# Kernel optimization log

Hardware: AMD Instinct MI355X
Metric: run time of the kernel (lower is better)

The kernel has to match this reference:

```python
import jax, jax.numpy as jnp
import numpy as np
from jax import lax

IN_DIM = 256
MID = IN_DIM // 2          # 128
NUM_FILTERS = 8
OUT_DIM = 256
EMBED_DIM = 256
BN_EPS = 1e-5


def star_relu(x, scale, bias):
    # StarReLU: s * relu(x)**2 + b
    return scale * jnp.square(jax.nn.relu(x)) + bias


def setup_inputs() -> dict:
    key = jax.random.key(0)
    ks = jax.random.split(key, 12)
    B, H, W = 2, 16, 16
    h, w = 128, 128
    inp = {
        "x": jax.random.normal(ks[0], (B, IN_DIM, H, W), jnp.float32),
        "y": jax.random.normal(ks[1], (B, OUT_DIM, h, w), jnp.float32),
        # feature_fuse: 1x1 conv, depthwise 3x3 conv, BatchNorm (eval-mode stats)
        "conv1_w": jax.random.normal(ks[2], (MID, IN_DIM), jnp.float32) * 0.02,
        "conv1_b": jnp.zeros((MID,), jnp.float32),
        "dw_w": jax.random.normal(ks[3], (MID, 3, 3), jnp.float32) * 0.02,
        "dw_b": jnp.zeros((MID,), jnp.float32),
        "bn_gamma": jnp.ones((MID,), jnp.float32),
        "bn_beta": jnp.zeros((MID,), jnp.float32),
        "bn_mean": jax.random.normal(ks[4], (MID,), jnp.float32) * 0.1,
        "bn_var": jax.random.uniform(ks[5], (MID,), jnp.float32, 0.5, 1.5),
        "sr1_scale": jnp.ones((1,), jnp.float32),
        "sr1_bias": jnp.zeros((1,), jnp.float32),
        # channle_expand 1x1 conv
        "ce_w": jax.random.normal(ks[6], (NUM_FILTERS, MID), jnp.float32) * 0.02,
        "ce_b": jnp.zeros((NUM_FILTERS,), jnp.float32),
        "sr2_scale": jnp.ones((1,), jnp.float32),
        "sr2_bias": jnp.zeros((1,), jnp.float32),
        "W_base": jax.random.normal(ks[7], (OUT_DIM * EMBED_DIM, NUM_FILTERS), jnp.float32) * 0.02,
    }
    return inp


def reference(x, y, conv1_w, conv1_b, dw_w, dw_b, bn_gamma, bn_beta, bn_mean,
              bn_var, sr1_scale, sr1_bias, ce_w, ce_b, sr2_scale, sr2_bias, W_base):
    B, _, fh, fw = x.shape
    b, c, h, w = y.shape
    ph, pw = h // fh, w // fw

    # feature_fuse
    t = jnp.einsum('bchw,oc->bohw', x, conv1_w) + conv1_b[None, :, None, None]
    t = lax.conv_general_dilated(
        t, dw_w[:, None, :, :], (1, 1), ((1, 1), (1, 1)),
        feature_group_count=MID,
        dimension_numbers=('NCHW', 'OIHW', 'NCHW')) + dw_b[None, :, None, None]
    t = bn_gamma[None, :, None, None] * (t - bn_mean[None, :, None, None]) \
        * lax.rsqrt(bn_var + BN_EPS)[None, :, None, None] + bn_beta[None, :, None, None]
    t = star_relu(t, sr1_scale, sr1_bias)

    # channle_expand + act -> per-location filter coefficients [b, F, fh, fw]
    wdec = star_relu(jnp.einsum('bchw,fc->bfhw', t, ce_w) + ce_b[None, :, None, None],
                     sr2_scale, sr2_bias)

    # hypernetwork: [b, E*O, fh, fw], flattened as (embed_dim, out_dim)
    Wd = jnp.einsum('bfhw,ef->behw', wdec, W_base)
    Wd = Wd.reshape(b, EMBED_DIM, OUT_DIM, fh, fw)

    # massive-group 1x1 conv == per-(batch, block) small GEMM over spatial patches
    yb = y.reshape(b, c, fh, ph, fw, pw)
    out = jnp.einsum('beoij,boipjq->beipjq', Wd, yb)  # [b, E, fh, ph, fw, pw]
    return out.reshape(b, EMBED_DIM, h, w)
```

## Files before the change

### kernel.cpp

```cpp
#include <hip/hip_runtime.h>
#include <stdint.h>

typedef unsigned short u16t;
typedef unsigned int   u32t;
typedef _Float16       h16;
typedef __attribute__((ext_vector_type(2))) _Float16 h16x2;
typedef __attribute__((ext_vector_type(8))) short short8;
typedef __attribute__((ext_vector_type(4))) float f32x4;

#if defined(__has_builtin)
#if __has_builtin(__builtin_amdgcn_fdot2)
#define HAVE_DOT2 1
#endif
#endif

__device__ __forceinline__ float dot2h(u32t a, u32t b, float c){
#ifdef HAVE_DOT2
  return __builtin_amdgcn_fdot2(__builtin_bit_cast(h16x2, a),
                                __builtin_bit_cast(h16x2, b), c, false);
#else
  h16x2 ha = __builtin_bit_cast(h16x2, a), hb = __builtin_bit_cast(h16x2, b);
  return c + (float)ha[0]*(float)hb[0] + (float)ha[1]*(float)hb[1];
#endif
}

__device__ __forceinline__ float bf2f(u16t h){
  union { u32t u; float f; } c; c.u = ((u32t)h) << 16; return c.f;
}
__device__ __forceinline__ u16t f2bf(float f){
  union { float f; u32t u; } c; c.f = f;
  u32t u = c.u;
  u = u + 0x7fffu + ((u >> 16) & 1u);
  return (u16t)(u >> 16);
}
__device__ __forceinline__ u32t pk2bf(float a, float b){
  return (u32t)f2bf(a) | ((u32t)f2bf(b) << 16);
}
__device__ __forceinline__ u32t pk2h(float a, float b){
  h16x2 h = { (h16)a, (h16)b };
  return __builtin_bit_cast(u32t, h);
}

template<bool BF>
__device__ __forceinline__ float ldv(const void* p, size_t i){
  if constexpr (BF) return bf2f(((const u16t*)p)[i]);
  else              return ((const float*)p)[i];
}
template<bool BF>
__device__ __forceinline__ void ld8(const void* p, size_t i, float* v){
  if constexpr (BF){
    uint4 u = *(const uint4*)((const u16t*)p + i);
    const u32t a[4] = {u.x, u.y, u.z, u.w};
#pragma unroll
    for (int d = 0; d < 4; ++d){
      v[2*d]   = bf2f((u16t)(a[d] & 0xffffu));
      v[2*d+1] = bf2f((u16t)(a[d] >> 16));
    }
  } else {
    const float4* q = (const float4*)((const float*)p + i);
    float4 A = q[0], B = q[1];
    v[0]=A.x; v[1]=A.y; v[2]=A.z; v[3]=A.w;
    v[4]=B.x; v[5]=B.y; v[6]=B.z; v[7]=B.w;
  }
}
template<bool BF>
__device__ __forceinline__ void ld8pk(const void* p, size_t i, u32t* dst){
  if constexpr (BF){
    uint4 u = *(const uint4*)((const u16t*)p + i);
    dst[0]=u.x; dst[1]=u.y; dst[2]=u.z; dst[3]=u.w;
  } else {
    const float4* q = (const float4*)((const float*)p + i);
    float4 A = q[0], B = q[1];
    dst[0] = pk2bf(A.x, A.y); dst[1] = pk2bf(A.z, A.w);
    dst[2] = pk2bf(B.x, B.y); dst[3] = pk2bf(B.z, B.w);
  }
}

__global__ void k_probe(const void* xv, int* flag){
  __shared__ int cnt;
  const int t = threadIdx.x;
  if (t == 0) cnt = 0;
  __syncthreads();
  u16t h = ((const u16t*)xv)[t];
  int e = (h >> 7) & 0xff;
  if (e >= 90 && e <= 150) atomicAdd(&cnt, 1);
  __syncthreads();
  if (t == 0) *flag = (cnt >= 104) ? 1 : 0;
}

template<bool BF>
__device__ __forceinline__ void pre12_body(
    const void* x, const void* w, const void* bias,
    const void* dww, const void* dwb,
    const void* bng, const void* bnb, const void* bnm, const void* bnv,
    const void* s1s, const void* s1b, float* t2)
{
  __shared__ float ts[2][256];
  const int cg = blockIdx.x, b = blockIdx.y;
  const int ij = threadIdx.x, i = ij >> 4, j = ij & 15;
  const int c0 = cg * 2;
  float a0 = ldv<BF>(bias, c0), a1 = ldv<BF>(bias, c0 + 1);
  const size_t xb = (size_t)b * 65536 + ij;
#pragma unroll 8
  for (int k = 0; k < 256; ++k){
    const float xv = ldv<BF>(x, xb + (size_t)k * 256);
    a0 += xv * ldv<BF>(w, (size_t)c0 * 256 + k);
    a1 += xv * ldv<BF>(w, (size_t)(c0 + 1) * 256 + k);
  }
  ts[0][ij] = a0;
  ts[1][ij] = a1;
  __syncthreads();
  const float sc1 = ldv<BF>(s1s, 0), sb1 = ldv<BF>(s1b, 0);
#pragma unroll
  for (int cc = 0; cc < 2; ++cc){
    const int c = c0 + cc;
    float s = ldv<BF>(dwb, c);
#pragma unroll
    for (int di = 0; di < 3; ++di){
      const int ii = i + di - 1;
      if (ii < 0 || ii > 15) continue;
#pragma unroll
      for (int dj = 0; dj < 3; ++dj){
        const int jj = j + dj - 1;
        if (jj < 0 || jj > 15) continue;
        s += ts[cc][ii * 16 + jj] * ldv<BF>(dww, c * 9 + di * 3 + dj);
      }
    }
    const float v = ldv<BF>(bng, c) * (s - ldv<BF>(bnm, c)) *
                    rsqrtf(ldv<BF>(bnv, c) + 1e-5f) + ldv<BF>(bnb, c);
    const float r = fmaxf(v, 0.0f);
    t2[((size_t)b * 128 + c) * 256 + ij] = sc1 * r * r + sb1;
  }
}
__global__ __launch_bounds__(256) void k_pre12(
    const void* x, const void* w, const void* bias,
    const void* dww, const void* dwb,
    const void* bng, const void* bnb, const void* bnm, const void* bnv,
    const void* s1s, const void* s1b, float* t2, const int* flag){
  if (*flag) pre12_body<true >(x,w,bias,dww,dwb,bng,bnb,bnm,bnv,s1s,s1b,t2);
  else       pre12_body<false>(x,w,bias,dww,dwb,bng,bnb,bnm,bnv,s1s,s1b,t2);
}

template<bool BF>
__device__ __forceinline__ void pre3_body(
    const float* t2, const void* cew, const void* ceb,
    const void* s2s, const void* s2b, float* wdecf, uint4* wdech)
{
  const int b = blockIdx.x, ij = threadIdx.x;
  float a[8];
#pragma unroll
  for (int f = 0; f < 8; ++f) a[f] = ldv<BF>(ceb, f);
#pragma unroll 4
  for (int c = 0; c < 128; ++c){
    const float tv = t2[((size_t)b * 128 + c) * 256 + ij];
#pragma unroll
    for (int f = 0; f < 8; ++f) a[f] += tv * ldv<BF>(cew, f * 128 + c);
  }
  const float sc2 = ldv<BF>(s2s, 0), sb2 = ldv<BF>(s2b, 0);
  float o[8];
#pragma unroll
  for (int f = 0; f < 8; ++f){
    const float r = fmaxf(a[f], 0.0f);
    o[f] = sc2 * r * r + sb2;
  }
  const int idx = b * 256 + ij;
#pragma unroll
  for (int f = 0; f < 8; ++f) wdecf[idx * 8 + f] = o[f];
  if (wdech){
    wdech[idx] = make_uint4(pk2h(o[0], o[1]), pk2h(o[2], o[3]),
                            pk2h(o[4], o[5]), pk2h(o[6], o[7]));
  }
}
__global__ __launch_bounds__(256) void k_pre3(
    const float* t2, const void* cew, const void* ceb,
    const void* s2s, const void* s2b, float* wdecf, uint4* wdech, const int* flag){
  if (*flag) pre3_body<true >(t2, cew, ceb, s2s, s2b, wdecf, wdech);
  else       pre3_body<false>(t2, cew, ceb, s2s, s2b, wdecf, wdech);
}

template<bool BF>
__device__ __forceinline__ void prew_body(const void* wb, uint4* wbh){
  const int t = blockIdx.x * 256 + threadIdx.x;
  float v[8];
  ld8<BF>(wb, (size_t)t * 8, v);
  wbh[t] = make_uint4(pk2h(v[0], v[1]), pk2h(v[2], v[3]),
                      pk2h(v[4], v[5]), pk2h(v[6], v[7]));
}
__global__ __launch_bounds__(256) void k_prew(const void* wb, uint4* wbh, const int* flag){
  if (*flag) prew_body<true >(wb, wbh);
  else       prew_body<false>(wb, wbh);
}

template<bool BF, bool PREW>
__device__ __forceinline__ void main_body(
    const void* y, const void* wbase, const uint4* wbh,
    const float* wdecf, const uint4* wdech, void* out, u16t* smem)
{
  const int gx  = blockIdx.x;
  const int ec  = blockIdx.y;
  const int b   = gx >> 6;
  const int i   = (gx >> 2) & 15;
  const int j0  = (gx & 3) * 4;
  const int tid = threadIdx.x;

  {
    const int o_oct = tid & 31;
    const int p     = (tid >> 5) & 7;
    const int gh    = tid >> 8;
#pragma unroll
    for (int gi = 0; gi < 2; ++gi){
      const int g = gh * 2 + gi;
      u32t Rp[8][4];
#pragma unroll
      for (int r = 0; r < 8; ++r){
        const size_t idx = (((size_t)(b * 256 + o_oct * 8 + r)) * 128 + (i * 8 + p)) * 128
                         + (j0 + g) * 8;
        ld8pk<BF>(y, idx, Rp[r]);
      }
#pragma unroll
      for (int q = 0; q < 8; ++q){
        const int d = q >> 1, h = q & 1;
        u32t cc[4];
#pragma unroll
        for (int k = 0; k < 4; ++k){
          const u32t lo32 = Rp[2*k][d], hi32 = Rp[2*k+1][d];
          cc[k] = h ? ((lo32 >> 16)     | (hi32 & 0xffff0000u))
                    : ((lo32 & 0xffffu) | (hi32 << 16));
        }
        const int row  = g * 64 + p * 8 + q;
        const int phys = (o_oct * 8 + row * 8) & 255;
        *(uint4*)(smem + row * 256 + phys) = make_uint4(cc[0], cc[1], cc[2], cc[3]);
      }
    }
  }
  __syncthreads();

  const int wave = tid >> 6, lane = tid & 63;
  const int l15 = lane & 15, l4 = lane >> 4;
  const int e0  = ec * 128 + wave * 16;
  const int e_a = e0 + l15;

  u32t wdp[4][4];
  float wdf[4][8];
#pragma unroll
  for (int g = 0; g < 4; ++g){
    const int loc = b * 256 + i * 16 + j0 + g;
    if constexpr (PREW){
      const uint4 q = wdech[loc];
      wdp[g][0] = q.x; wdp[g][1] = q.y; wdp[g][2] = q.z; wdp[g][3] = q.w;
    } else {
#pragma unroll
      for (int f = 0; f < 8; ++f) wdf[g][f] = wdecf[loc * 8 + f];
    }
  }

  f32x4 acc[4][4];
#pragma unroll
  for (int g = 0; g < 4; ++g)
#pragma unroll
    for (int nt = 0; nt < 4; ++nt)
      acc[g][nt] = (f32x4){0.f, 0.f, 0.f, 0.f};

  const uint4* wb4 = wbh + (size_t)e_a * 256 + l4 * 8;
  const size_t wb_off = (size_t)e_a * 2048 + (size_t)l4 * 64;

  u32t Wb[2][8][4];
#pragma unroll
  for (int m = 0; m < 8; ++m){
    if constexpr (PREW){
      const uint4 q = wb4[m];
      Wb[0][m][0]=q.x; Wb[0][m][1]=q.y; Wb[0][m][2]=q.z; Wb[0][m][3]=q.w;
    } else {
      ld8pk<BF>(wbase, wb_off + m * 8, Wb[0][m]);
    }
  }

#pragma unroll
  for (int ks = 0; ks < 8; ++ks){
    const int cur = ks & 1;
    if (ks < 7){
#pragma unroll
      for (int m = 0; m < 8; ++m){
        if constexpr (PREW){
          const uint4 q = wb4[(ks + 1) * 32 + m];
          Wb[cur^1][m][0]=q.x; Wb[cur^1][m][1]=q.y; Wb[cur^1][m][2]=q.z; Wb[cur^1][m][3]=q.w;
        } else {
          ld8pk<BF>(wbase, wb_off + (size_t)(ks + 1) * 256 + m * 8, Wb[cur^1][m]);
        }
      }
    }
    float s[4][8];
#pragma unroll
    for (int m = 0; m < 8; ++m){
      if constexpr (PREW){
#pragma unroll
        for (int g = 0; g < 4; ++g){
          float t = 0.f;
#pragma unroll
          for (int d = 0; d < 4; ++d) t = dot2h(Wb[cur][m][d], wdp[g][d], t);
          s[g][m] = t;
        }
      } else {
        float wf[8];
#pragma unroll
        for (int d = 0; d < 4; ++d){
          wf[2*d]   = bf2f((u16t)(Wb[cur][m][d] & 0xffffu));
          wf[2*d+1] = bf2f((u16t)(Wb[cur][m][d] >> 16));
        }
#pragma unroll
        for (int g = 0; g < 4; ++g){
          float t = 0.f;
#pragma unroll
          for (int f = 0; f < 8; ++f) t += wf[f] * wdf[g][f];
          s[g][m] = t;
        }
      }
    }
#pragma unroll
    for (int g = 0; g < 4; ++g){
      short8 af;
#pragma unroll
      for (int m = 0; m < 8; ++m) af[m] = (short)f2bf(s[g][m]);
#pragma unroll
      for (int nt = 0; nt < 4; ++nt){
        const int row = g * 64 + nt * 16 + l15;
        const int c0  = (ks * 32 + l4 * 8 + row * 8) & 255;
        const short8 bfr = *(const short8*)(smem + row * 256 + c0);
        acc[g][nt] = __builtin_amdgcn_mfma_f32_16x16x32_bf16(af, bfr, acc[g][nt], 0, 0, 0);
      }
    }
  }

#pragma unroll
  for (int g = 0; g < 4; ++g){
#pragma unroll
    for (int nt = 0; nt < 4; ++nt){
      const int col = nt * 16 + l15;
      const int pp = col >> 3, qq = col & 7;
#pragma unroll
      for (int r = 0; r < 4; ++r){
        const int ee = e0 + l4 * 4 + r;
        const size_t oaddr = ((size_t)(b * 256 + ee) * 128 + (i * 8 + pp)) * 128
                           + (j0 + g) * 8 + qq;
        const float v = acc[g][nt][r];
        if constexpr (BF) ((u16t*)out)[oaddr] = f2bf(v);
        else              ((float*)out)[oaddr] = v;
      }
    }
  }
}

__global__ __launch_bounds__(512, 2) void k_main_pw(
    const void* y, const uint4* wbh, const uint4* wdech, void* out, const int* flag){
  extern __shared__ __align__(16) u16t smem[];
  if (*flag) main_body<true , true>(y, nullptr, wbh, nullptr, wdech, out, smem);
  else       main_body<false, true>(y, nullptr, wbh, nullptr, wdech, out, smem);
}
__global__ __launch_bounds__(512, 2) void k_main_npw(
    const void* y, const void* wbase, const float* wdecf, void* out, const int* flag){
  extern __shared__ __align__(16) u16t smem[];
  if (*flag) main_body<true , false>(y, wbase, nullptr, wdecf, nullptr, out, smem);
  else       main_body<false, false>(y, wbase, nullptr, wdecf, nullptr, out, smem);
}

extern "C" void kernel_launch(void* const* d_in, const int* in_sizes, int n_in,
                              void* d_out, int out_size, void* d_ws, size_t ws_size,
                              hipStream_t stream)
{
  float* t2    = (float*)d_ws;
  float* wdecf = (float*)((char*)d_ws + 262144);
  int*   flag  = (int*)((char*)d_ws + 278528);
  uint4* wdech = (uint4*)((char*)d_ws + 278544);
  uint4* wbh   = (uint4*)((char*)d_ws + 286736);
  const bool prew = (ws_size >= 286736u + 1048576u);

  k_probe<<<dim3(1), dim3(128), 0, stream>>>(d_in[0], flag);
  k_pre12<<<dim3(64, 2), dim3(256), 0, stream>>>(
      d_in[0], d_in[2], d_in[3], d_in[4], d_in[5], d_in[6], d_in[7],
      d_in[8], d_in[9], d_in[10], d_in[11], t2, flag);
  k_pre3<<<dim3(2), dim3(256), 0, stream>>>(
      t2, d_in[12], d_in[13], d_in[14], d_in[15], wdecf,
      prew ? wdech : (uint4*)nullptr, flag);

  const int lds_bytes = 4 * 64 * 256 * 2;
  if (prew){
    k_prew<<<dim3(256), dim3(256), 0, stream>>>(d_in[16], wbh, flag);
    hipFuncSetAttribute((const void*)k_main_pw,
                        hipFuncAttributeMaxDynamicSharedMemorySize, lds_bytes);
    k_main_pw<<<dim3(128, 2), dim3(512), lds_bytes, stream>>>(
        d_in[1], wbh, wdech, d_out, flag);
  } else {
    hipFuncSetAttribute((const void*)k_main_npw,
                        hipFuncAttributeMaxDynamicSharedMemorySize, lds_bytes);
    k_main_npw<<<dim3(128, 2), dim3(512), lds_bytes, stream>>>(
        d_in[1], d_in[16], wdecf, d_out, flag);
  }
}
```

Measured before the change: 179.5 us.

## Rework main GEMM to 32x32 MFMA with 1024-thread blocks and inline dtype probe

The main kernel now runs 1024 threads per block, with each thread staging one spatial group, and uses 32x32x16 bf16 MFMA tiles in place of 16x16x32. The LDS swizzle and the per-wave work split (4 groups by 4 embed tiles) are restructured, and the double-buffered W prefetch is dropped. The separate probe kernel is replaced by a ballot-based check inside each kernel. The non-prewidened fallback path goes away, along with the bf16 output path, and the pre12 kernel now runs one channel per block. Bf16 packing uses a perm-based rounding that is cheaper but no longer round-to-nearest-even, and the workspace-size check is gone, so a large enough workspace is assumed.

After: 210.8 us. +17.5%, slower.

```diff
diff --git a/kernel.cpp b/kernel.cpp
--- a/kernel.cpp
+++ b/kernel.cpp
@@ -4,9 +4,9 @@
 typedef unsigned short u16t;
 typedef unsigned int   u32t;
 typedef _Float16       h16;
-typedef __attribute__((ext_vector_type(2))) _Float16 h16x2;
-typedef __attribute__((ext_vector_type(8))) short short8;
-typedef __attribute__((ext_vector_type(4))) float f32x4;
+typedef __attribute__((ext_vector_type(2)))  _Float16 h16x2;
+typedef __attribute__((ext_vector_type(8)))  short    short8;
+typedef __attribute__((ext_vector_type(16))) float    f32x16;
 
 #if defined(__has_builtin)
 #if __has_builtin(__builtin_amdgcn_fdot2)
@@ -27,14 +27,10 @@
 __device__ __forceinline__ float bf2f(u16t h){
   union { u32t u; float f; } c; c.u = ((u32t)h) << 16; return c.f;
 }
-__device__ __forceinline__ u16t f2bf(float f){
-  union { float f; u32t u; } c; c.f = f;
-  u32t u = c.u;
-  u = u + 0x7fffu + ((u >> 16) & 1u);
-  return (u16t)(u >> 16);
-}
 __device__ __forceinline__ u32t pk2bf(float a, float b){
-  return (u32t)f2bf(a) | ((u32t)f2bf(b) << 16);
+  u32t ua = __builtin_bit_cast(u32t, a) + 0x8000u;
+  u32t ub = __builtin_bit_cast(u32t, b) + 0x8000u;
+  return __builtin_amdgcn_perm(ub, ua, 0x07060302u);
 }
 __device__ __forceinline__ u32t pk2h(float a, float b){
   h16x2 h = { (h16)a, (h16)b };
@@ -76,16 +72,14 @@
   }
 }
 
-__global__ void k_probe(const void* xv, int* flag){
-  __shared__ int cnt;
-  const int t = threadIdx.x;
-  if (t == 0) cnt = 0;
-  __syncthreads();
-  u16t h = ((const u16t*)xv)[t];
-  int e = (h >> 7) & 0xff;
-  if (e >= 90 && e <= 150) atomicAdd(&cnt, 1);
-  __syncthreads();
-  if (t == 0) *flag = (cnt >= 104) ? 1 : 0;
+__device__ __forceinline__ bool probe_bf(const void* xv){
+  const u16t* p = (const u16t*)xv;
+  const int lane = threadIdx.x & 63;
+  const u16t h0 = p[lane], h1 = p[lane + 64];
+  const int e0 = (h0 >> 7) & 0xff, e1 = (h1 >> 7) & 0xff;
+  unsigned long long b0 = __ballot(e0 >= 90 && e0 <= 150);
+  unsigned long long b1 = __ballot(e1 >= 90 && e1 <= 150);
+  return (__popcll(b0) + __popcll(b1)) >= 104;
 }
 
 template<bool BF>
@@ -95,58 +89,54 @@
     const void* bng, const void* bnb, const void* bnm, const void* bnv,
     const void* s1s, const void* s1b, float* t2)
 {
-  __shared__ float ts[2][256];
-  const int cg = blockIdx.x, b = blockIdx.y;
+  __shared__ float ts[256];
+  const int bid = blockIdx.x;
+  const int b = bid >> 7, c = bid & 127;
   const int ij = threadIdx.x, i = ij >> 4, j = ij & 15;
-  const int c0 = cg * 2;
-  float a0 = ldv<BF>(bias, c0), a1 = ldv<BF>(bias, c0 + 1);
+  float a0 = ldv<BF>(bias, c);
   const size_t xb = (size_t)b * 65536 + ij;
 #pragma unroll 8
-  for (int k = 0; k < 256; ++k){
-    const float xv = ldv<BF>(x, xb + (size_t)k * 256);
-    a0 += xv * ldv<BF>(w, (size_t)c0 * 256 + k);
-    a1 += xv * ldv<BF>(w, (size_t)(c0 + 1) * 256 + k);
-  }
-  ts[0][ij] = a0;
-  ts[1][ij] = a1;
+  for (int k = 0; k < 256; ++k)
+    a0 += ldv<BF>(x, xb + (size_t)k * 256) * ldv<BF>(w, (size_t)c * 256 + k);
+  ts[ij] = a0;
   __syncthreads();
-  const float sc1 = ldv<BF>(s1s, 0), sb1 = ldv<BF>(s1b, 0);
-#pragma unroll
-  for (int cc = 0; cc < 2; ++cc){
-    const int c = c0 + cc;
-    float s = ldv<BF>(dwb, c);
-#pragma unroll
-    for (int di = 0; di < 3; ++di){
-      const int ii = i + di - 1;
-      if (ii < 0 || ii > 15) continue;
-#pragma unroll
-      for (int dj = 0; dj < 3; ++dj){
-        const int jj = j + dj - 1;
-        if (jj < 0 || jj > 15) continue;
-        s += ts[cc][ii * 16 + jj] * ldv<BF>(dww, c * 9 + di * 3 + dj);
-      }
-    }
-    const float v = ldv<BF>(bng, c) * (s - ldv<BF>(bnm, c)) *
-                    rsqrtf(ldv<BF>(bnv, c) + 1e-5f) + ldv<BF>(bnb, c);
-    const float r = fmaxf(v, 0.0f);
-    t2[((size_t)b * 128 + c) * 256 + ij] = sc1 * r * r + sb1;
-  }
+  float s = ldv<BF>(dwb, c);
+#pragma unroll
+  for (int di = 0; di < 3; ++di){
+    const int ii = i + di - 1;
+    if (ii < 0 || ii > 15) continue;
+#pragma unroll
+    for (int dj = 0; dj < 3; ++dj){
+      const int jj = j + dj - 1;
+      if (jj < 0 || jj > 15) continue;
+      s += ts[ii * 16 + jj] * ldv<BF>(dww, c * 9 + di * 3 + dj);
+    }
+  }
+  const float v = ldv<BF>(bng, c) * (s - ldv<BF>(bnm, c)) *
+                  rsqrtf(ldv<BF>(bnv, c) + 1e-5f) + ldv<BF>(bnb, c);
+  const float r = fmaxf(v, 0.0f);
+  t2[((size_t)b * 128 + c) * 256 + ij] = ldv<BF>(s1s, 0) * r * r + ldv<BF>(s1b, 0);
 }
 __global__ __launch_bounds__(256) void k_pre12(
     const void* x, const void* w, const void* bias,
     const void* dww, const void* dwb,
     const void* bng, const void* bnb, const void* bnm, const void* bnv,
-    const void* s1s, const void* s1b, float* t2, const int* flag){
-  if (*flag) pre12_body<true >(x,w,bias,dww,dwb,bng,bnb,bnm,bnv,s1s,s1b,t2);
-  else       pre12_body<false>(x,w,bias,dww,dwb,bng,bnb,bnm,bnv,s1s,s1b,t2);
+    const void* s1s, const void* s1b, float* t2){
+  if (probe_bf(x)) pre12_body<true >(x,w,bias,dww,dwb,bng,bnb,bnm,bnv,s1s,s1b,t2);
+  else             pre12_body<false>(x,w,bias,dww,dwb,bng,bnb,bnm,bnv,s1s,s1b,t2);
 }
 
 template<bool BF>
 __device__ __forceinline__ void pre3_body(
-    const float* t2, const void* cew, const void* ceb,
-    const void* s2s, const void* s2b, float* wdecf, uint4* wdech)
+    const void* x, const float* t2, const void* cew, const void* ceb,
+    const void* s2s, const void* s2b, uint4* wdech)
 {
+  __shared__ float cs[8][128];
   const int b = blockIdx.x, ij = threadIdx.x;
+  {
+    for (int t = ij; t < 1024; t += 256) cs[t >> 7][t & 127] = ldv<BF>(cew, t);
+  }
+  __syncthreads();
   float a[8];
 #pragma unroll
   for (int f = 0; f < 8; ++f) a[f] = ldv<BF>(ceb, f);
@@ -154,7 +144,7 @@
   for (int c = 0; c < 128; ++c){
     const float tv = t2[((size_t)b * 128 + c) * 256 + ij];
 #pragma unroll
-    for (int f = 0; f < 8; ++f) a[f] += tv * ldv<BF>(cew, f * 128 + c);
+    for (int f = 0; f < 8; ++f) a[f] += tv * cs[f][c];
   }
   const float sc2 = ldv<BF>(s2s, 0), sb2 = ldv<BF>(s2b, 0);
   float o[8];
@@ -163,19 +153,14 @@
     const float r = fmaxf(a[f], 0.0f);
     o[f] = sc2 * r * r + sb2;
   }
-  const int idx = b * 256 + ij;
-#pragma unroll
-  for (int f = 0; f < 8; ++f) wdecf[idx * 8 + f] = o[f];
-  if (wdech){
-    wdech[idx] = make_uint4(pk2h(o[0], o[1]), pk2h(o[2], o[3]),
-                            pk2h(o[4], o[5]), pk2h(o[6], o[7]));
-  }
+  wdech[b * 256 + ij] = make_uint4(pk2h(o[0], o[1]), pk2h(o[2], o[3]),
+                                   pk2h(o[4], o[5]), pk2h(o[6], o[7]));
 }
 __global__ __launch_bounds__(256) void k_pre3(
-    const float* t2, const void* cew, const void* ceb,
-    const void* s2s, const void* s2b, float* wdecf, uint4* wdech, const int* flag){
-  if (*flag) pre3_body<true >(t2, cew, ceb, s2s, s2b, wdecf, wdech);
-  else       pre3_body<false>(t2, cew, ceb, s2s, s2b, wdecf, wdech);
+    const void* x, const float* t2, const void* cew, const void* ceb,
+    const void* s2s, const void* s2b, uint4* wdech){
+  if (probe_bf(x)) pre3_body<true >(x, t2, cew, ceb, s2s, s2b, wdech);
+  else             pre3_body<false>(x, t2, cew, ceb, s2s, s2b, wdech);
 }
 
 template<bool BF>
@@ -186,15 +171,14 @@
   wbh[t] = make_uint4(pk2h(v[0], v[1]), pk2h(v[2], v[3]),
                       pk2h(v[4], v[5]), pk2h(v[6], v[7]));
 }
-__global__ __launch_bounds__(256) void k_prew(const void* wb, uint4* wbh, const int* flag){
-  if (*flag) prew_body<true >(wb, wbh);
-  else       prew_body<false>(wb, wbh);
-}
-
-template<bool BF, bool PREW>
+__global__ __launch_bounds__(256) void k_prew(const void* x, const void* wb, uint4* wbh){
+  if (probe_bf(x)) prew_body<true >(wb, wbh);
+  else             prew_body<false>(wb, wbh);
+}
+
+template<bool BF>
 __device__ __forceinline__ void main_body(
-    const void* y, const void* wbase, const uint4* wbh,
-    const float* wdecf, const uint4* wdech, void* out, u16t* smem)
+    const void* y, const uint4* wbh, const uint4* wdech, float* out, u16t* smem)
 {
   const int gx  = blockIdx.x;
   const int ec  = blockIdx.y;
@@ -206,161 +190,95 @@
   {
     const int o_oct = tid & 31;
     const int p     = (tid >> 5) & 7;
-    const int gh    = tid >> 8;
-#pragma unroll
-    for (int gi = 0; gi < 2; ++gi){
-      const int g = gh * 2 + gi;
-      u32t Rp[8][4];
-#pragma unroll
-      for (int r = 0; r < 8; ++r){
-        const size_t idx = (((size_t)(b * 256 + o_oct * 8 + r)) * 128 + (i * 8 + p)) * 128
-                         + (j0 + g) * 8;
-        ld8pk<BF>(y, idx, Rp[r]);
+    const int g     = tid >> 8;
+    u32t Rp[8][4];
+#pragma unroll
+    for (int r = 0; r < 8; ++r){
+      const size_t idx = (((size_t)(b * 256 + o_oct * 8 + r)) * 128 + (i * 8 + p)) * 128
+                       + (j0 + g) * 8;
+      ld8pk<BF>(y, idx, Rp[r]);
+    }
+#pragma unroll
+    for (int q = 0; q < 8; ++q){
+      const int d = q >> 1, h = q & 1;
+      u32t cc[4];
+#pragma unroll
+      for (int k = 0; k < 4; ++k){
+        const u32t lo32 = Rp[2*k][d], hi32 = Rp[2*k+1][d];
+        cc[k] = h ? ((lo32 >> 16)     | (hi32 & 0xffff0000u))
+                  : ((lo32 & 0xffffu) | (hi32 << 16));
       }
-#pragma unroll
-      for (int q = 0; q < 8; ++q){
-        const int d = q >> 1, h = q & 1;
-        u32t cc[4];
-#pragma unroll
-        for (int k = 0; k < 4; ++k){
-          const u32t lo32 = Rp[2*k][d], hi32 = Rp[2*k+1][d];
-          cc[k] = h ? ((lo32 >> 16)     | (hi32 & 0xffff0000u))
-                    : ((lo32 & 0xffffu) | (hi32 << 16));
-        }
-        const int row  = g * 64 + p * 8 + q;
-        const int phys = (o_oct * 8 + row * 8) & 255;
-        *(uint4*)(smem + row * 256 + phys) = make_uint4(cc[0], cc[1], cc[2], cc[3]);
-      }
+      const int row  = g * 64 + p * 8 + q;
+      const int phys = (o_oct + row) & 31;
+      *(uint4*)(smem + row * 256 + phys * 8) = make_uint4(cc[0], cc[1], cc[2], cc[3]);
     }
   }
   __syncthreads();
 
   const int wave = tid >> 6, lane = tid & 63;
-  const int l15 = lane & 15, l4 = lane >> 4;
-  const int e0  = ec * 128 + wave * 16;
-  const int e_a = e0 + l15;
-
-  u32t wdp[4][4];
-  float wdf[4][8];
-#pragma unroll
-  for (int g = 0; g < 4; ++g){
-    const int loc = b * 256 + i * 16 + j0 + g;
-    if constexpr (PREW){
-      const uint4 q = wdech[loc];
-      wdp[g][0] = q.x; wdp[g][1] = q.y; wdp[g][2] = q.z; wdp[g][3] = q.w;
-    } else {
-#pragma unroll
-      for (int f = 0; f < 8; ++f) wdf[g][f] = wdecf[loc * 8 + f];
-    }
-  }
-
-  f32x4 acc[4][4];
-#pragma unroll
-  for (int g = 0; g < 4; ++g)
-#pragma unroll
-    for (int nt = 0; nt < 4; ++nt)
-      acc[g][nt] = (f32x4){0.f, 0.f, 0.f, 0.f};
-
-  const uint4* wb4 = wbh + (size_t)e_a * 256 + l4 * 8;
-  const size_t wb_off = (size_t)e_a * 2048 + (size_t)l4 * 64;
-
-  u32t Wb[2][8][4];
-#pragma unroll
-  for (int m = 0; m < 8; ++m){
-    if constexpr (PREW){
-      const uint4 q = wb4[m];
-      Wb[0][m][0]=q.x; Wb[0][m][1]=q.y; Wb[0][m][2]=q.z; Wb[0][m][3]=q.w;
-    } else {
-      ld8pk<BF>(wbase, wb_off + m * 8, Wb[0][m]);
-    }
-  }
-
-#pragma unroll
-  for (int ks = 0; ks < 8; ++ks){
-    const int cur = ks & 1;
-    if (ks < 7){
-#pragma unroll
-      for (int m = 0; m < 8; ++m){
-        if constexpr (PREW){
-          const uint4 q = wb4[(ks + 1) * 32 + m];
-          Wb[cur^1][m][0]=q.x; Wb[cur^1][m][1]=q.y; Wb[cur^1][m][2]=q.z; Wb[cur^1][m][3]=q.w;
-        } else {
-          ld8pk<BF>(wbase, wb_off + (size_t)(ks + 1) * 256 + m * 8, Wb[cur^1][m]);
-        }
-      }
-    }
-    float s[4][8];
-#pragma unroll
-    for (int m = 0; m < 8; ++m){
-      if constexpr (PREW){
-#pragma unroll
-        for (int g = 0; g < 4; ++g){
-          float t = 0.f;
-#pragma unroll
-          for (int d = 0; d < 4; ++d) t = dot2h(Wb[cur][m][d], wdp[g][d], t);
-          s[g][m] = t;
-        }
-      } else {
-        float wf[8];
-#pragma unroll
-        for (int d = 0; d < 4; ++d){
-          wf[2*d]   = bf2f((u16t)(Wb[cur][m][d] & 0xffffu));
-          wf[2*d+1] = bf2f((u16t)(Wb[cur][m][d] >> 16));
-        }
-#pragma unroll
-        for (int g = 0; g < 4; ++g){
-          float t = 0.f;
-#pragma unroll
-          for (int f = 0; f < 8; ++f) t += wf[f] * wdf[g][f];
-          s[g][m] = t;
-        }
-      }
-    }
-#pragma unroll
-    for (int g = 0; g < 4; ++g){
-      short8 af;
-#pragma unroll
-      for (int m = 0; m < 8; ++m) af[m] = (short)f2bf(s[g][m]);
-#pragma unroll
-      for (int nt = 0; nt < 4; ++nt){
-        const int row = g * 64 + nt * 16 + l15;
-        const int c0  = (ks * 32 + l4 * 8 + row * 8) & 255;
-        const short8 bfr = *(const short8*)(smem + row * 256 + c0);
-        acc[g][nt] = __builtin_amdgcn_mfma_f32_16x16x32_bf16(af, bfr, acc[g][nt], 0, 0, 0);
-      }
-    }
-  }
-
-#pragma unroll
-  for (int g = 0; g < 4; ++g){
-#pragma unroll
-    for (int nt = 0; nt < 4; ++nt){
-      const int col = nt * 16 + l15;
-      const int pp = col >> 3, qq = col & 7;
-#pragma unroll
-      for (int r = 0; r < 4; ++r){
-        const int ee = e0 + l4 * 4 + r;
-        const size_t oaddr = ((size_t)(b * 256 + ee) * 128 + (i * 8 + pp)) * 128
-                           + (j0 + g) * 8 + qq;
-        const float v = acc[g][nt][r];
-        if constexpr (BF) ((u16t*)out)[oaddr] = f2bf(v);
-        else              ((float*)out)[oaddr] = v;
-      }
-    }
-  }
-}
-
-__global__ __launch_bounds__(512, 2) void k_main_pw(
-    const void* y, const uint4* wbh, const uint4* wdech, void* out, const int* flag){
+  const int g    = wave & 3, et = wave >> 2;
+  const int n31  = lane & 31, kh = lane >> 5;
+  const int e0   = ec * 128 + et * 32;
+  const int e_a  = e0 + n31;
+
+  u32t wdp[4];
+  {
+    const uint4 q = wdech[b * 256 + i * 16 + j0 + g];
+    wdp[0] = q.x; wdp[1] = q.y; wdp[2] = q.z; wdp[3] = q.w;
+  }
+
+  f32x16 acc[2];
+#pragma unroll
+  for (int nt = 0; nt < 2; ++nt)
+#pragma unroll
+    for (int k = 0; k < 16; ++k) acc[nt][k] = 0.0f;
+
+  const uint4* wrow = wbh + (size_t)e_a * 256 + kh * 8;
+
+#pragma unroll
+  for (int ks = 0; ks < 16; ++ks){
+    uint4 Wq[8];
+#pragma unroll
+    for (int r = 0; r < 8; ++r) Wq[r] = wrow[ks * 16 + r];
+    float s[8];
+#pragma unroll
+    for (int r = 0; r < 8; ++r){
+      float t = dot2h(Wq[r].x, wdp[0], 0.0f);
+      t = dot2h(Wq[r].y, wdp[1], t);
+      t = dot2h(Wq[r].z, wdp[2], t);
+      s[r] = dot2h(Wq[r].w, wdp[3], t);
+    }
+    u32t a4[4];
+#pragma unroll
+    for (int d = 0; d < 4; ++d) a4[d] = pk2bf(s[2*d], s[2*d+1]);
+    const short8 af = __builtin_bit_cast(short8, *(uint4*)a4);
+#pragma unroll
+    for (int nt = 0; nt < 2; ++nt){
+      const int rowf = g * 64 + nt * 32 + n31;
+      const int phys = (2 * ks + kh + rowf) & 31;
+      const short8 bfr = *(const short8*)(smem + rowf * 256 + phys * 8);
+      acc[nt] = __builtin_amdgcn_mfma_f32_32x32x16_bf16(af, bfr, acc[nt], 0, 0, 0);
+    }
+  }
+
+#pragma unroll
+  for (int nt = 0; nt < 2; ++nt){
+    const int pq = nt * 32 + n31;
+    const int pp = pq >> 3, qq = pq & 7;
+    const size_t obase = ((size_t)(b * 256) * 128 + (i * 8 + pp)) * 128
+                       + (j0 + g) * 8 + qq;
+#pragma unroll
+    for (int r = 0; r < 16; ++r){
+      const int ee = e0 + (r & 3) + 8 * (r >> 2) + 4 * kh;
+      out[obase + (size_t)ee * 16384] = acc[nt][r];
+    }
+  }
+}
+__global__ __launch_bounds__(1024, 4) void k_main(
+    const void* x, const void* y, const uint4* wbh, const uint4* wdech, float* out){
   extern __shared__ __align__(16) u16t smem[];
-  if (*flag) main_body<true , true>(y, nullptr, wbh, nullptr, wdech, out, smem);
-  else       main_body<false, true>(y, nullptr, wbh, nullptr, wdech, out, smem);
-}
-__global__ __launch_bounds__(512, 2) void k_main_npw(
-    const void* y, const void* wbase, const float* wdecf, void* out, const int* flag){
-  extern __shared__ __align__(16) u16t smem[];
-  if (*flag) main_body<true , false>(y, wbase, nullptr, wdecf, nullptr, out, smem);
-  else       main_body<false, false>(y, wbase, nullptr, wdecf, nullptr, out, smem);
+  if (probe_bf(x)) main_body<true >(y, wbh, wdech, out, smem);
+  else             main_body<false>(y, wbh, wdech, out, smem);
 }
 
 extern "C" void kernel_launch(void* const* d_in, const int* in_sizes, int n_in,
@@ -368,31 +286,19 @@
                               hipStream_t stream)
 {
   float* t2    = (float*)d_ws;
-  float* wdecf = (float*)((char*)d_ws + 262144);
-  int*   flag  = (int*)((char*)d_ws + 278528);
-  uint4* wdech = (uint4*)((char*)d_ws + 278544);
-  uint4* wbh   = (uint4*)((char*)d_ws + 286736);
-  const bool prew = (ws_size >= 286736u + 1048576u);
-
-  k_probe<<<dim3(1), dim3(128), 0, stream>>>(d_in[0], flag);
-  k_pre12<<<dim3(64, 2), dim3(256), 0, stream>>>(
+  uint4* wdech = (uint4*)((char*)d_ws + 262144);
+  uint4* wbh   = (uint4*)((char*)d_ws + 270336);
+
+  k_pre12<<<dim3(256), dim3(256), 0, stream>>>(
       d_in[0], d_in[2], d_in[3], d_in[4], d_in[5], d_in[6], d_in[7],
-      d_in[8], d_in[9], d_in[10], d_in[11], t2, flag);
+      d_in[8], d_in[9], d_in[10], d_in[11], t2);
   k_pre3<<<dim3(2), dim3(256), 0, stream>>>(
-      t2, d_in[12], d_in[13], d_in[14], d_in[15], wdecf,
-      prew ? wdech : (uint4*)nullptr, flag);
+      d_in[0], t2, d_in[12], d_in[13], d_in[14], d_in[15], wdech);
+  k_prew<<<dim3(256), dim3(256), 0, stream>>>(d_in[0], d_in[16], wbh);
 
   const int lds_bytes = 4 * 64 * 256 * 2;
-  if (prew){
-    k_prew<<<dim3(256), dim3(256), 0, stream>>>(d_in[16], wbh, flag);
-    hipFuncSetAttribute((const void*)k_main_pw,
-                        hipFuncAttributeMaxDynamicSharedMemorySize, lds_bytes);
-    k_main_pw<<<dim3(128, 2), dim3(512), lds_bytes, stream>>>(
-        d_in[1], wbh, wdech, d_out, flag);
-  } else {
-    hipFuncSetAttribute((const void*)k_main_npw,
-                        hipFuncAttributeMaxDynamicSharedMemorySize, lds_bytes);
-    k_main_npw<<<dim3(128, 2), dim3(512), lds_bytes, stream>>>(
-        d_in[1], d_in[16], wdecf, d_out, flag);
-  }
-}
+  hipFuncSetAttribute((const void*)k_main,
+                      hipFuncAttributeMaxDynamicSharedMemorySize, lds_bytes);
+  k_main<<<dim3(128, 2), dim3(1024), lds_bytes, stream>>>(
+      d_in[0], d_in[1], wbh, wdech, (float*)d_out);
+}
```
